# Kernel tuning notes

Hardware: AMD Instinct MI355X
Metric: run time of the kernel (lower is better)

Reference implementation:

```python
import jax, jax.numpy as jnp
import numpy as np
from math import pi

N = 20000        # nodes
E = 640000       # edges (avg degree 32)
H = 128          # hidden_channels = num_filters
NB = 3           # num_bond_features
NGS = 50 - NB    # gaussians in smearing (num_gaussians - num_bond_features)
CUT = 10.0       # cutoff
L = 3            # num_interactions
B = 16           # graphs in batch
LOG2 = 0.6931471805599453


def ssp(x):
    # ShiftedSoftplus
    return jax.nn.softplus(x) - LOG2


def setup_inputs() -> dict:
    key = jax.random.key(0)
    ks = jax.random.split(key, 20)
    s = 0.05
    inp = {
        "z": jax.random.randint(ks[0], (N,), 0, 100),
        "pos": jax.random.uniform(ks[1], (N, 3), jnp.float32),
        "batch": jnp.sort(jax.random.randint(ks[2], (N,), 0, B)),
        "edge_index": jax.random.randint(ks[3], (2, E), 0, N),
        "edge_attr": jax.random.uniform(ks[4], (E, NB), jnp.float32),
        # parameters (stacked over L interaction blocks where per-layer)
        "emb": jax.random.normal(ks[5], (100, H), jnp.float32) * s,
        "mlp_w1": jax.random.normal(ks[6], (L, NB + NGS, H), jnp.float32) * s,
        "mlp_b1": jnp.zeros((L, H), jnp.float32),
        "mlp_w2": jax.random.normal(ks[7], (L, H, H), jnp.float32) * s,
        "mlp_b2": jnp.zeros((L, H), jnp.float32),
        "cf1_w": jax.random.normal(ks[8], (L, H, H), jnp.float32) * s,   # lin1, no bias
        "cf2_w": jax.random.normal(ks[9], (L, H, H), jnp.float32) * s,
        "cf2_b": jnp.zeros((L, H), jnp.float32),
        "lin_w": jax.random.normal(ks[10], (L, H, H), jnp.float32) * s,
        "lin_b": jnp.zeros((L, H), jnp.float32),
        "out1_w": jax.random.normal(ks[11], (H, H // 2), jnp.float32) * s,
        "out1_b": jnp.zeros((H // 2,), jnp.float32),
        "out2_w": jax.random.normal(ks[12], (H // 2, 1), jnp.float32) * s,
        "out2_b": jnp.zeros((1,), jnp.float32),
    }
    return inp


def reference(z, pos, batch, edge_index, edge_attr, emb,
              mlp_w1, mlp_b1, mlp_w2, mlp_b2,
              cf1_w, cf2_w, cf2_b, lin_w, lin_b,
              out1_w, out1_b, out2_w, out2_b):
    row, col = edge_index[0], edge_index[1]  # source j, target i
    h = emb[z]                               # [N,H] embedding_e(z)
    # edge_weight = ||pos[row] - pos[col]||
    ew = jnp.linalg.norm(pos[row] - pos[col], axis=-1)  # [E]
    # GaussianSmearing(0, cutoff, NGS)
    offset = jnp.linspace(0.0, CUT, NGS, dtype=jnp.float32)
    coeff = -0.5 / (offset[1] - offset[0]) ** 2
    gs = jnp.exp(coeff * (ew[:, None] - offset[None, :]) ** 2)  # [E,NGS]
    ea = jnp.concatenate([edge_attr, gs], axis=1)  # [E,50]
    # cosine cutoff weight
    C = 0.5 * (jnp.cos(ew * pi / CUT) + 1.0)       # [E]
    for l in range(L):
        # filter MLP on edge features
        W = ssp(ea @ mlp_w1[l] + mlp_b1[l]) @ mlp_w2[l] + mlp_b2[l]  # [E,H]
        W = W * C[:, None]
        xh = h @ cf1_w[l]                    # lin1 (no bias) [N,H]
        msg = xh[row] * W                    # gather-mul [E,H]
        agg = jax.ops.segment_sum(msg, col, num_segments=N)  # scatter-add [N,H]
        xc = agg @ cf2_w[l] + cf2_b[l]       # lin2
        xc = ssp(xc)
        xc = xc @ lin_w[l] + lin_b[l]        # block output lin
        h = h + xc                           # residual
    h = ssp(h @ out1_w + out1_b)             # [N,H/2]
    per_node = h @ out2_w + out2_b           # [N,1]
    out = jax.ops.segment_sum(per_node, batch, num_segments=B)  # readout 'add' -> [B,1]
    return out
```

## Files before the change

### kernel.cpp

```cpp
#include <hip/hip_runtime.h>
#include <hip/hip_bf16.h>

typedef __attribute__((ext_vector_type(8))) short bfrag;
typedef __attribute__((ext_vector_type(4))) float f32x4;

__device__ __forceinline__ float ssp_f(float x) {
    return fmaxf(x, 0.f) + __logf(1.f + __expf(-fabsf(x))) - 0.6931471805599453f;
}

__device__ __forceinline__ unsigned short f2b(float x) {
    __hip_bfloat16 h = __float2bfloat16(x);
    return *(unsigned short*)&h;
}

__device__ __forceinline__ unsigned int pk2(float a, float b) {
    __hip_bfloat162 h2 = __float22bfloat162_rn(make_float2(a, b));
    return *(unsigned int*)&h2;
}

__device__ __forceinline__ void stage32x128(
    const float* __restrict__ src, long r0, int N, int t, short (*dst)[136])
{
    #pragma unroll
    for (int j = 0; j < 4; ++j) {
        const int fi = t + j * 256;
        const int r = fi >> 5, c4 = (fi & 31) << 2;
        const long n = r0 + r;
        float4 v = make_float4(0.f, 0.f, 0.f, 0.f);
        if (n < N) v = *(const float4*)(src + n * 128 + c4);
        *(uint2*)&dst[r][c4] = make_uint2(pk2(v.x, v.y), pk2(v.z, v.w));
    }
}

__global__ void sniff_kernel(const unsigned int* __restrict__ raw, int* __restrict__ flag)
{
    __shared__ int cnt[256];
    const int t = threadIdx.x;
    unsigned int w = raw[t];
    unsigned int e = (w >> 7) & 0xFFu;
    cnt[t] = (e >= 100u && e <= 135u) ? 1 : 0;
    __syncthreads();
    for (int s = 128; s > 0; s >>= 1) {
        if (t < s) cnt[t] += cnt[t + s];
        __syncthreads();
    }
    if (t == 0) *flag = (cnt[0] >= 160) ? 1 : 0;
}

__global__ void sniff_int_kernel(const unsigned int* __restrict__ z, int* __restrict__ iflag)
{
    __shared__ int cnt[128];
    const int t = threadIdx.x;
    cnt[t] = (z[2 * t + 1] == 0u) ? 1 : 0;
    __syncthreads();
    for (int s = 64; s > 0; s >>= 1) {
        if (t < s) cnt[t] += cnt[t + s];
        __syncthreads();
    }
    if (t == 0) *iflag = (cnt[0] >= 126) ? 1 : 0;
}

struct Cvt16 {
    const void* src[16];
    long off[17];
};

__global__ __launch_bounds__(256) void convert_fused_kernel(
    Cvt16 args, float* __restrict__ F, long total, const int* __restrict__ flag)
{
    long i = (long)blockIdx.x * 256 + threadIdx.x;
    if (i >= total) return;
    int lo = 0, hi = 16;
    while (hi - lo > 1) {
        int mid = (lo + hi) >> 1;
        if (i >= args.off[mid]) lo = mid; else hi = mid;
    }
    long loc = i - args.off[lo];
    if (*flag) F[i] = __bfloat162float(((const __hip_bfloat16*)args.src[lo])[loc]);
    else       F[i] = ((const float*)args.src[lo])[loc];
}

__global__ __launch_bounds__(256) void convert_int_kernel(
    const void* __restrict__ src, int* __restrict__ dst, int n,
    const int* __restrict__ iflag)
{
    int i = blockIdx.x * 256 + threadIdx.x;
    if (i >= n) return;
    if (*iflag) dst[i] = (int)(((const long long*)src)[i]);
    else        dst[i] = ((const int*)src)[i];
}

__global__ __launch_bounds__(256) void embed_kernel(
    const int* __restrict__ z, const float* __restrict__ embf,
    float* __restrict__ h, int NH)
{
    int idx = blockIdx.x * 256 + threadIdx.x;
    if (idx >= NH) return;
    h[idx] = embf[z[idx >> 7] * 128 + (idx & 127)];
}

__global__ __launch_bounds__(256) void zero_int_kernel(int* p, int n)
{
    int i = blockIdx.x * 256 + threadIdx.x;
    if (i < n) p[i] = 0;
}

__global__ __launch_bounds__(256) void hist_kernel(const int* __restrict__ col,
                                                   int* __restrict__ count, int E)
{
    int e = blockIdx.x * 256 + threadIdx.x;
    if (e < E) atomicAdd(&count[col[e]], 1);
}

__global__ __launch_bounds__(256) void scan_kernel(const int* __restrict__ count,
                                                   int* __restrict__ rowptr,
                                                   int* __restrict__ next, int N)
{
    __shared__ int part[256];
    const int t = threadIdx.x;
    const int chunk = (N + 255) / 256;
    const int lo = t * chunk, hi = min(lo + chunk, N);
    int s = 0;
    for (int i = lo; i < hi; ++i) s += count[i];
    part[t] = s;
    __syncthreads();
    if (t == 0) {
        int run = 0;
        for (int i = 0; i < 256; ++i) { int v = part[i]; part[i] = run; run += v; }
        rowptr[N] = run;
    }
    __syncthreads();
    int run = part[t];
    for (int i = lo; i < hi; ++i) {
        rowptr[i] = run; next[i] = run;
        run += count[i];
    }
}

__global__ __launch_bounds__(256) void prep_scatter_kernel(
    const float* __restrict__ posf, const int* __restrict__ row,
    const int* __restrict__ col, const float* __restrict__ eattrf,
    int* __restrict__ next,
    int* __restrict__ rowS, int* __restrict__ colS,
    float* __restrict__ CS, float* __restrict__ ewS,
    unsigned short* __restrict__ eaS, int E, int NB)
{
    int e = blockIdx.x * 256 + threadIdx.x;
    if (e >= E) return;
    const int r = row[e], c = col[e];
    const int p = atomicAdd(&next[c], 1);
    float dx = posf[r*3+0] - posf[c*3+0];
    float dy = posf[r*3+1] - posf[c*3+1];
    float dz = posf[r*3+2] - posf[c*3+2];
    float ew = sqrtf(dx*dx + dy*dy + dz*dz);
    rowS[p] = r; colS[p] = c; ewS[p] = ew;
    CS[p] = 0.5f * (cosf(ew * 0.3141592653589793f) + 1.0f);
    unsigned short* o = eaS + (long)p * 4;
    for (int q = 0; q < 4; ++q)
        o[q] = (q < NB) ? f2b(eattrf[(long)e * NB + q]) : (unsigned short)0;
}

__global__ __launch_bounds__(256) void wtrans_kernel(
    const float* __restrict__ src, unsigned short* __restrict__ dst,
    int K, int Kpad, int N)
{
    int idx = blockIdx.x * 256 + threadIdx.x;
    if (idx >= N * Kpad) return;
    int n = idx / Kpad, k = idx - n * Kpad;
    dst[idx] = (k < K) ? f2b(src[k * N + n]) : (unsigned short)0;
}

__global__ __launch_bounds__(256) void wtrans_node_kernel(
    const float* __restrict__ cf1, const float* __restrict__ cf2,
    const float* __restrict__ lin, unsigned short* __restrict__ dst, int total)
{
    int idx = blockIdx.x * 256 + threadIdx.x;
    if (idx >= total) return;
    int m = idx >> 14;
    int fam = m % 3, l = m / 3;
    int local = idx & 16383;
    int n = local >> 7, k = local & 127;
    const float* src = (fam == 0 ? cf1 : fam == 1 ? cf2 : lin) + (long)l * 16384;
    dst[idx] = f2b(src[k * 128 + n]);
}

template<int MODE>
__global__ __launch_bounds__(256) void node_gemm_tiled(
    const float* __restrict__ in, const float* __restrict__ W,
    const float* __restrict__ bias, float* __restrict__ out, int N)
{
    __shared__ float in_s[32][128];
    const int t = threadIdx.x;
    const long n0 = (long)blockIdx.x * 32;
    for (int i = t; i < 32 * 128; i += 256) {
        long n = n0 + (i >> 7);
        in_s[i >> 7][i & 127] = (n < N) ? in[n * 128 + (i & 127)] : 0.f;
    }
    __syncthreads();
    const int j = t & 31, sub = t >> 5;
    const int c4 = j * 4, rb = sub * 4;
    float acc[4][4];
    float4 bv = make_float4(0.f, 0.f, 0.f, 0.f);
    if (MODE != 0) bv = *(const float4*)(bias + c4);
    #pragma unroll
    for (int i = 0; i < 4; ++i) { acc[i][0]=bv.x; acc[i][1]=bv.y; acc[i][2]=bv.z; acc[i][3]=bv.w; }
    #pragma unroll 4
    for (int k = 0; k < 128; ++k) {
        const float4 wv = *(const float4*)(W + k * 128 + c4);
        #pragma unroll
        for (int i = 0; i < 4; ++i) {
            const float a = in_s[rb + i][k];
            acc[i][0] += a * wv.x; acc[i][1] += a * wv.y;
            acc[i][2] += a * wv.z; acc[i][3] += a * wv.w;
        }
    }
    #pragma unroll
    for (int i = 0; i < 4; ++i) {
        long n = n0 + rb + i;
        if (n >= N) continue;
        float4 o;
        if (MODE == 1) {
            o.x = ssp_f(acc[i][0]); o.y = ssp_f(acc[i][1]);
            o.z = ssp_f(acc[i][2]); o.w = ssp_f(acc[i][3]);
        } else {
            o.x = acc[i][0]; o.y = acc[i][1]; o.z = acc[i][2]; o.w = acc[i][3];
        }
        if (MODE == 2) {
            float4 p = *(const float4*)(out + n * 128 + c4);
            o.x += p.x; o.y += p.y; o.z += p.z; o.w += p.w;
        }
        *(float4*)(out + n * 128 + c4) = o;
    }
}

__global__ __launch_bounds__(256) void node_gemm1_mfma(
    const float* __restrict__ in, const unsigned short* __restrict__ wt,
    float* __restrict__ out, float* __restrict__ aggz, int N)
{
    __shared__ __align__(16) short a_b[32][136];
    const int t = threadIdx.x;
    const long r0 = (long)blockIdx.x * 32;
    stage32x128(in, r0, N, t, a_b);
    {
        const float4 z = make_float4(0.f, 0.f, 0.f, 0.f);
        #pragma unroll
        for (int j = 0; j < 4; ++j) {
            const int fi = t + j * 256;
            const long n = r0 + (fi >> 5);
            if (n < N) *(float4*)(aggz + n * 128 + ((fi & 31) << 2)) = z;
        }
    }
    __syncthreads();
    const int lane = t & 63, w = t >> 6;
    const int colL = lane & 15, quad = lane >> 4;
    const int rt = (w & 1) * 16 + colL;
    const int nh = (w >> 1) * 64;
    f32x4 acc[4];
    #pragma unroll
    for (int tt = 0; tt < 4; ++tt) acc[tt] = (f32x4){0.f, 0.f, 0.f, 0.f};
    #pragma unroll
    for (int ks = 0; ks < 4; ++ks) {
        const bfrag a = *(const bfrag*)&a_b[rt][ks * 32 + quad * 8];
        #pragma unroll
        for (int tt = 0; tt < 4; ++tt) {
            const bfrag wf = *(const bfrag*)&wt[(long)(nh + tt * 16 + colL) * 128 + ks * 32 + quad * 8];
            acc[tt] = __builtin_amdgcn_mfma_f32_16x16x32_bf16(wf, a, acc[tt], 0, 0, 0);
        }
    }
    const long node = r0 + rt;
    if (node < N) {
        float* orow = out + node * 128;
        #pragma unroll
        for (int tt = 0; tt < 4; ++tt) {
            const int c0 = nh + tt * 16 + quad * 4;
            *(float4*)(orow + c0) = make_float4(acc[tt][0], acc[tt][1], acc[tt][2], acc[tt][3]);
        }
    }
}

template<int CHAIN>
__global__ __launch_bounds__(256) void node_gemm23_mfma(
    const float* __restrict__ in,
    const unsigned short* __restrict__ w1t, const float* __restrict__ b1,
    const unsigned short* __restrict__ w2t, const float* __restrict__ b2,
    float* __restrict__ h,
    const unsigned short* __restrict__ cf1t, float* __restrict__ xh,
    float* __restrict__ aggz, int N)
{
    __shared__ __align__(16) short a_b[32][136];
    __shared__ __align__(16) short t_b[32][136];
    const int t = threadIdx.x;
    const long r0 = (long)blockIdx.x * 32;
    stage32x128(in, r0, N, t, a_b);
    __syncthreads();
    const int lane = t & 63, w = t >> 6;
    const int colL = lane & 15, quad = lane >> 4;
    const int rt = (w & 1) * 16 + colL;
    const int nh = (w >> 1) * 64;
    {
        f32x4 acc[4];
        #pragma unroll
        for (int tt = 0; tt < 4; ++tt) acc[tt] = (f32x4){0.f, 0.f, 0.f, 0.f};
        #pragma unroll
        for (int ks = 0; ks < 4; ++ks) {
            const bfrag a = *(const bfrag*)&a_b[rt][ks * 32 + quad * 8];
            #pragma unroll
            for (int tt = 0; tt < 4; ++tt) {
                const bfrag wf = *(const bfrag*)&w1t[(long)(nh + tt * 16 + colL) * 128 + ks * 32 + quad * 8];
                acc[tt] = __builtin_amdgcn_mfma_f32_16x16x32_bf16(wf, a, acc[tt], 0, 0, 0);
            }
        }
        #pragma unroll
        for (int tt = 0; tt < 4; ++tt) {
            const int c0 = nh + tt * 16 + quad * 4;
            const float4 bv = *(const float4*)(b1 + c0);
            const float v0 = ssp_f(acc[tt][0] + bv.x);
            const float v1 = ssp_f(acc[tt][1] + bv.y);
            const float v2 = ssp_f(acc[tt][2] + bv.z);
            const float v3 = ssp_f(acc[tt][3] + bv.w);
            *(uint2*)&t_b[rt][c0] = make_uint2(pk2(v0, v1), pk2(v2, v3));
        }
    }
    __syncthreads();
    {
        f32x4 acc[4];
        #pragma unroll
        for (int tt = 0; tt < 4; ++tt) acc[tt] = (f32x4){0.f, 0.f, 0.f, 0.f};
        #pragma unroll
        for (int ks = 0; ks < 4; ++ks) {
            const bfrag a = *(const bfrag*)&t_b[rt][ks * 32 + quad * 8];
            #pragma unroll
            for (int tt = 0; tt < 4; ++tt) {
                const bfrag wf = *(const bfrag*)&w2t[(long)(nh + tt * 16 + colL) * 128 + ks * 32 + quad * 8];
                acc[tt] = __builtin_amdgcn_mfma_f32_16x16x32_bf16(wf, a, acc[tt], 0, 0, 0);
            }
        }
        const long node = r0 + rt;
        if (node < N) {
            float* hrow = h + node * 128;
            #pragma unroll
            for (int tt = 0; tt < 4; ++tt) {
                const int c0 = nh + tt * 16 + quad * 4;
                const float4 bv = *(const float4*)(b2 + c0);
                float4 hv = *(const float4*)(hrow + c0);
                hv.x += acc[tt][0] + bv.x;
                hv.y += acc[tt][1] + bv.y;
                hv.z += acc[tt][2] + bv.z;
                hv.w += acc[tt][3] + bv.w;
                *(float4*)(hrow + c0) = hv;
                if (CHAIN)
                    *(uint2*)&a_b[rt][c0] = make_uint2(pk2(hv.x, hv.y), pk2(hv.z, hv.w));
            }
        }
    }
    if (CHAIN) {
        __syncthreads();
        f32x4 acc[4];
        #pragma unroll
        for (int tt = 0; tt < 4; ++tt) acc[tt] = (f32x4){0.f, 0.f, 0.f, 0.f};
        #pragma unroll
        for (int ks = 0; ks < 4; ++ks) {
            const bfrag a = *(const bfrag*)&a_b[rt][ks * 32 + quad * 8];
            #pragma unroll
            for (int tt = 0; tt < 4; ++tt) {
                const bfrag wf = *(const bfrag*)&cf1t[(long)(nh + tt * 16 + colL) * 128 + ks * 32 + quad * 8];
                acc[tt] = __builtin_amdgcn_mfma_f32_16x16x32_bf16(wf, a, acc[tt], 0, 0, 0);
            }
        }
        const long node = r0 + rt;
        if (node < N) {
            float* orow = xh + node * 128;
            float* zrow = aggz + node * 128;
            const float4 z = make_float4(0.f, 0.f, 0.f, 0.f);
            #pragma unroll
            for (int tt = 0; tt < 4; ++tt) {
                const int c0 = nh + tt * 16 + quad * 4;
                *(float4*)(orow + c0) = make_float4(acc[tt][0], acc[tt][1], acc[tt][2], acc[tt][3]);
                *(float4*)(zrow + c0) = z;
            }
        }
    }
}

__global__ __launch_bounds__(256, 8) void edge_mfma(
    const int* __restrict__ rowS, const int* __restrict__ colS,
    const float* __restrict__ CS, const float* __restrict__ ewS,
    const unsigned short* __restrict__ eaS,
    const unsigned short* __restrict__ w1t, const float* __restrict__ b1,
    const unsigned short* __restrict__ w2t, const float* __restrict__ b2,
    const float* __restrict__ xh, float* __restrict__ agg,
    int E, int NB, int F50, float delta, float coeff)
{
    __shared__ __align__(16) char smem[32 * 132 * 4];
    short (*ea_b)[64]    = (short(*)[64])smem;
    short (*t_b)[128]    = (short(*)[128])(smem + 4096);
    float (*runbuf)[132] = (float(*)[132])smem;
    __shared__ int   row_s[32];
    __shared__ int   col_s[32];
    __shared__ float C_s[32];
    __shared__ float ew_s[32];

    const int t = threadIdx.x;
    const long p0 = (long)blockIdx.x * 32;

    {
        const int t32 = t & 31;
        long p = p0 + t32; if (p >= E) p = E - 1;
        row_s[t32] = rowS[p];
        col_s[t32] = colS[p];
        C_s[t32]   = (p0 + t32 < E) ? CS[p] : 0.f;
        ew_s[t32]  = ewS[p];
    }
    for (int i = t; i < 32 * 64; i += 256) {
        const int e = i >> 6, k = i & 63;
        long p = p0 + e; if (p >= E) p = E - 1;
        unsigned short v;
        if (k < NB)        v = eaS[p * 4 + k];
        else if (k < F50) {
            float d = ew_s[e] - (float)(k - NB) * delta;
            v = f2b(__expf(coeff * d * d));
        } else             v = 0;
        ea_b[e][k ^ ((e & 7) << 3)] = (short)v;
    }
    __syncthreads();

    const int lane = t & 63;
    const int w    = t >> 6;
    const int colL = lane & 15;
    const int quad = lane >> 4;
    const int m0   = (w & 1) * 16;
    const int ebase = m0 + quad * 4;

    float xv[4][4];

    {
        f32x4 acc[4];
        #pragma unroll
        for (int tt = 0; tt < 4; ++tt) acc[tt] = (f32x4){0.f, 0.f, 0.f, 0.f};
        const int ar  = m0 + colL;
        const int asw = (ar & 7) << 3;
        #pragma unroll
        for (int ks = 0; ks < 2; ++ks) {
            const bfrag a = *(const bfrag*)&ea_b[ar][(ks * 32 + quad * 8) ^ asw];
            #pragma unroll
            for (int tt = 0; tt < 4; ++tt) {
                const int n0 = ((w >> 1) * 4 + tt) * 16;
                const bfrag b = *(const bfrag*)&w1t[(long)(n0 + colL) * 64 + ks * 32 + quad * 8];
                acc[tt] = __builtin_amdgcn_mfma_f32_16x16x32_bf16(a, b, acc[tt], 0, 0, 0);
            }
        }
        #pragma unroll
        for (int reg = 0; reg < 4; ++reg) {
            const float* xr = xh + (long)row_s[ebase + reg] * 128;
            #pragma unroll
            for (int tt = 0; tt < 4; ++tt)
                xv[reg][tt] = xr[((w >> 1) * 4 + tt) * 16 + colL];
        }
        #pragma unroll
        for (int tt = 0; tt < 4; ++tt) {
            const int n0 = ((w >> 1) * 4 + tt) * 16;
            const float bcol = b1[n0 + colL];
            #pragma unroll
            for (int reg = 0; reg < 4; ++reg) {
                const int rr = m0 + quad * 4 + reg;
                float v = ssp_f(acc[tt][reg] + bcol);
                t_b[rr][(n0 + colL) ^ ((rr & 7) << 3)] = (short)f2b(v);
            }
        }
    }
    __syncthreads();

    {
        f32x4 acc[4];
        #pragma unroll
        for (int tt = 0; tt < 4; ++tt) acc[tt] = (f32x4){0.f, 0.f, 0.f, 0.f};
        const int ar  = m0 + colL;
        const int asw = (ar & 7) << 3;
        #pragma unroll
        for (int ks = 0; ks < 4; ++ks) {
            const bfrag a = *(const bfrag*)&t_b[ar][(ks * 32 + quad * 8) ^ asw];
            #pragma unroll
            for (int tt = 0; tt < 4; ++tt) {
                const int n0 = ((w >> 1) * 4 + tt) * 16;
                const bfrag b = *(const bfrag*)&w2t[(long)(n0 + colL) * 128 + ks * 32 + quad * 8];
                acc[tt] = __builtin_amdgcn_mfma_f32_16x16x32_bf16(a, b, acc[tt], 0, 0, 0);
            }
        }
        __syncthreads();
        #pragma unroll
        for (int tt = 0; tt < 4; ++tt) {
            const int n0 = ((w >> 1) * 4 + tt) * 16;
            const int cg = n0 + colL;
            const float bcol = b2[cg];
            #pragma unroll
            for (int reg = 0; reg < 4; ++reg) {
                const int e = ebase + reg;
                const float v = acc[tt][reg] + bcol;
                runbuf[e][cg] = v * C_s[e] * xv[reg][tt];
            }
        }
    }
    __syncthreads();

    {
        const int cc   = t & 127;
        const int e0h  = (t >> 7) * 16;
        float a     = runbuf[e0h][cc];
        int  curcol = col_s[e0h];
        #pragma unroll 4
        for (int e = e0h + 1; e < e0h + 16; ++e) {
            const int c2 = col_s[e];
            if (c2 != curcol) {
                atomicAdd(&agg[(long)curcol * 128 + cc], a);
                a = 0.f; curcol = c2;
            }
            a += runbuf[e][cc];
        }
        atomicAdd(&agg[(long)curcol * 128 + cc], a);
    }
}

__global__ __launch_bounds__(256) void edge_atomic(
    const float* __restrict__ posf,
    const int* __restrict__ row, const int* __restrict__ col,
    const float* __restrict__ eattrf,
    const float* __restrict__ w1, const float* __restrict__ b1,
    const float* __restrict__ w2, const float* __restrict__ b2,
    const float* __restrict__ xh, float* __restrict__ agg,
    int E, int NB, int F50, float delta, float coeff)
{
    __shared__ float ea_s[32][52];
    __shared__ float t_s[32][128];
    __shared__ int   row_s[32];
    __shared__ int   col_s[32];
    __shared__ float C_s[32];
    __shared__ float ew_s[32];

    const int t = threadIdx.x;
    const long e0 = (long)blockIdx.x * 32;

    if (t < 32) {
        long e = e0 + t; if (e >= E) e = E - 1;
        const int r = row[e], c = col[e];
        row_s[t] = r; col_s[t] = c;
        float dx = posf[r*3+0] - posf[c*3+0];
        float dy = posf[r*3+1] - posf[c*3+1];
        float dz = posf[r*3+2] - posf[c*3+2];
        float ew = sqrtf(dx*dx + dy*dy + dz*dz);
        ew_s[t] = ew;
        C_s[t]  = (e0 + t < E) ? 0.5f * (cosf(ew * 0.3141592653589793f) + 1.0f) : 0.f;
        for (int q = 0; q < NB; ++q)
            ea_s[t][q] = eattrf[e * NB + q];
    }
    __syncthreads();
    {
        const int NGS = F50 - NB;
        for (int i = t; i < 32 * NGS; i += 256) {
            const int e = i / NGS, g = i - e * NGS;
            const float d = ew_s[e] - (float)g * delta;
            ea_s[e][NB + g] = __expf(coeff * d * d);
        }
    }
    __syncthreads();

    const int j = t & 31, sub = t >> 5;
    const int c4 = j * 4, eb = sub * 4;
    float acc[4][4];
    {
        const float4 bv = *(const float4*)(b1 + c4);
        #pragma unroll
        for (int i = 0; i < 4; ++i) { acc[i][0]=bv.x; acc[i][1]=bv.y; acc[i][2]=bv.z; acc[i][3]=bv.w; }
        for (int k = 0; k < F50; ++k) {
            const float4 wv = *(const float4*)(w1 + k * 128 + c4);
            #pragma unroll
            for (int i = 0; i < 4; ++i) {
                const float a = ea_s[eb + i][k];
                acc[i][0] += a * wv.x; acc[i][1] += a * wv.y;
                acc[i][2] += a * wv.z; acc[i][3] += a * wv.w;
            }
        }
        #pragma unroll
        for (int i = 0; i < 4; ++i) {
            float4 o;
            o.x = ssp_f(acc[i][0]); o.y = ssp_f(acc[i][1]);
            o.z = ssp_f(acc[i][2]); o.w = ssp_f(acc[i][3]);
            *(float4*)&t_s[eb + i][c4] = o;
        }
    }
    __syncthreads();
    {
        const float4 bv = *(const float4*)(b2 + c4);
        #pragma unroll
        for (int i = 0; i < 4; ++i) { acc[i][0]=bv.x; acc[i][1]=bv.y; acc[i][2]=bv.z; acc[i][3]=bv.w; }
        #pragma unroll 4
        for (int k = 0; k < 128; ++k) {
            const float4 wv = *(const float4*)(w2 + k * 128 + c4);
            #pragma unroll
            for (int i = 0; i < 4; ++i) {
                const float a = t_s[eb + i][k];
                acc[i][0] += a * wv.x; acc[i][1] += a * wv.y;
                acc[i][2] += a * wv.z; acc[i][3] += a * wv.w;
            }
        }
    }
    #pragma unroll
    for (int i = 0; i < 4; ++i) {
        const int e = eb + i;
        if (e0 + e >= E) continue;
        const float Ce = C_s[e];
        const float4 xv = *(const float4*)(xh + (long)row_s[e] * 128 + c4);
        float* ag = agg + (long)col_s[e] * 128 + c4;
        atomicAdd(ag + 0, acc[i][0] * Ce * xv.x);
        atomicAdd(ag + 1, acc[i][1] * Ce * xv.y);
        atomicAdd(ag + 2, acc[i][2] * Ce * xv.z);
        atomicAdd(ag + 3, acc[i][3] * Ce * xv.w);
    }
}

__global__ __launch_bounds__(256) void readout_mfma(
    const float* __restrict__ h, const unsigned short* __restrict__ o1t,
    const float* __restrict__ o1b, const float* __restrict__ o2w,
    const float* __restrict__ o2b, const int* __restrict__ batch,
    float* __restrict__ accb, int N)
{
    __shared__ __align__(16) short a_b[32][136];
    __shared__ float nb[32];
    const int t = threadIdx.x;
    const long r0 = (long)blockIdx.x * 32;
    stage32x128(h, r0, N, t, a_b);
    if (t < 32) nb[t] = 0.f;
    __syncthreads();
    const int lane = t & 63, w = t >> 6;
    const int colL = lane & 15, quad = lane >> 4;
    const int rt = (w & 1) * 16 + colL;
    const int nh = (w >> 1) * 32;
    f32x4 acc[2];
    #pragma unroll
    for (int tt = 0; tt < 2; ++tt) acc[tt] = (f32x4){0.f, 0.f, 0.f, 0.f};
    #pragma unroll
    for (int ks = 0; ks < 4; ++ks) {
        const bfrag a = *(const bfrag*)&a_b[rt][ks * 32 + quad * 8];
        #pragma unroll
        for (int tt = 0; tt < 2; ++tt) {
            const bfrag wf = *(const bfrag*)&o1t[(long)(nh + tt * 16 + colL) * 128 + ks * 32 + quad * 8];
            acc[tt] = __builtin_amdgcn_mfma_f32_16x16x32_bf16(wf, a, acc[tt], 0, 0, 0);
        }
    }
    float s = 0.f;
    #pragma unroll
    for (int tt = 0; tt < 2; ++tt) {
        const int c0 = nh + tt * 16 + quad * 4;
        const float4 bv = *(const float4*)(o1b + c0);
        const float4 wv = *(const float4*)(o2w + c0);
        s += ssp_f(acc[tt][0] + bv.x) * wv.x;
        s += ssp_f(acc[tt][1] + bv.y) * wv.y;
        s += ssp_f(acc[tt][2] + bv.z) * wv.z;
        s += ssp_f(acc[tt][3] + bv.w) * wv.w;
    }
    s += __shfl_xor(s, 16);
    s += __shfl_xor(s, 32);
    if (quad == 0) atomicAdd(&nb[rt], s);
    __syncthreads();
    if (t < 32) {
        const long node = r0 + t;
        if (node < N) atomicAdd(&accb[batch[node]], nb[t] + o2b[0]);
    }
}

__global__ __launch_bounds__(128) void readout_simple(
    const float* __restrict__ h,
    const float* __restrict__ o1w, const float* __restrict__ o1b,
    const float* __restrict__ o2w, const float* __restrict__ o2b,
    const int* __restrict__ batch, float* __restrict__ accb)
{
    __shared__ float hr[128];
    __shared__ float vv[64];
    const int n = blockIdx.x;
    const int t = threadIdx.x;
    hr[t] = h[(long)n * 128 + t];
    __syncthreads();
    if (t < 64) {
        float a = o1b[t];
        #pragma unroll 8
        for (int k = 0; k < 128; ++k)
            a = fmaf(hr[k], o1w[k * 64 + t], a);
        vv[t] = ssp_f(a) * o2w[t];
    }
    __syncthreads();
    if (t < 32) vv[t] += vv[t + 32];
    __syncthreads();
    if (t < 16) vv[t] += vv[t + 16];
    __syncthreads();
    if (t < 8)  vv[t] += vv[t + 8];
    __syncthreads();
    if (t < 4)  vv[t] += vv[t + 4];
    __syncthreads();
    if (t < 2)  vv[t] += vv[t + 2];
    __syncthreads();
    if (t == 0) atomicAdd(&accb[batch[n]], vv[0] + vv[1] + o2b[0]);
}

__global__ void finalize_kernel(const float* __restrict__ accb,
                                float* __restrict__ out, int B)
{
    int t = blockIdx.x * 256 + threadIdx.x;
    if (t < B) out[t] = accb[t];
}

extern "C" void kernel_launch(void* const* d_in, const int* in_sizes, int n_in,
                              void* d_out, int out_size, void* d_ws, size_t ws_size,
                              hipStream_t stream)
{
    const int N   = in_sizes[0];
    const int E   = in_sizes[3] / 2;
    const int B   = out_size;
    const int H   = 128;
    const int L   = in_sizes[7] / H;
    const int NB  = in_sizes[4] / E;
    const int F50 = in_sizes[6] / (L * H);
    const int NGS = F50 - NB;
    const float delta = 10.0f / (float)(NGS - 1);
    const float coeff = -0.5f / (delta * delta);

    const int fidx[16] = {1, 4, 5, 6, 7, 8, 9, 10, 11, 12, 13, 14, 15, 16, 17, 18};
    Cvt16 cv;
    cv.off[0] = 0;
    for (int i = 0; i < 16; ++i) {
        cv.src[i] = d_in[fidx[i]];
        cv.off[i + 1] = cv.off[i] + in_sizes[fidx[i]];
    }
    const long ftot = cv.off[16];

    float* F = (float*)d_ws;
    long base = (ftot + 3) & ~3L;
    float* h    = F + base;
    float* xh   = h + (long)N * H;
    float* agg  = xh + (long)N * H;
    float* accb = agg + (long)N * H;
    int*   flag  = (int*)(accb + ((B + 3) & ~3));
    int*   iflag = flag + 1;
    int*   zi     = flag + 4;
    int*   batchi = zi + N;
    int*   eidxi  = batchi + N;
    int*   count  = eidxi + 2 * E;
    int*   rowptr = count + N;
    int*   next   = rowptr + N + 1;
    int*   rowS   = next + N;
    int*   colS   = rowS + E;
    float* CS     = (float*)(colS + E);
    float* ewS    = CS + E;
    unsigned short* eaS = (unsigned short*)(ewS + E);
    unsigned short* w1t = eaS + 4L * E;
    unsigned short* w2t = w1t + (long)L * 128 * 64;
    unsigned short* nwt = w2t + (long)L * 128 * 128;
    unsigned short* o1t = nwt + 3L * L * 128 * 128;
    long used_bytes = (long)((char*)(o1t + 64 * 128) - (char*)d_ws);
    const bool use_fast = (used_bytes <= (long)ws_size) && (F50 <= 64) && (NB <= 4);

    sniff_kernel<<<1, 256, 0, stream>>>((const unsigned int*)d_in[5], flag);
    sniff_int_kernel<<<1, 128, 0, stream>>>((const unsigned int*)d_in[0], iflag);

    convert_fused_kernel<<<(int)((ftot + 255) / 256), 256, 0, stream>>>(cv, F, ftot, flag);
    convert_int_kernel<<<(N + 255) / 256, 256, 0, stream>>>(d_in[0], zi, N, iflag);
    convert_int_kernel<<<(N + 255) / 256, 256, 0, stream>>>(d_in[2], batchi, N, iflag);
    convert_int_kernel<<<(2 * E + 255) / 256, 256, 0, stream>>>(d_in[3], eidxi, 2 * E, iflag);

    const float* posf   = F + cv.off[0];
    const float* eattrf = F + cv.off[1];
    const float* embf   = F + cv.off[2];
    const float* w1   = F + cv.off[3];  const float* b1   = F + cv.off[4];
    const float* w2   = F + cv.off[5];  const float* b2   = F + cv.off[6];
    const float* cf1  = F + cv.off[7];  const float* cf2  = F + cv.off[8];
    const float* cf2b = F + cv.off[9];  const float* lin  = F + cv.off[10];
    const float* linb = F + cv.off[11]; const float* o1   = F + cv.off[12];
    const float* o1b  = F + cv.off[13]; const float* o2   = F + cv.off[14];
    const float* o2b  = F + cv.off[15];

    if (use_fast) {
        zero_int_kernel<<<(N + 255) / 256, 256, 0, stream>>>(count, N);
        hist_kernel<<<(E + 255) / 256, 256, 0, stream>>>(eidxi + E, count, E);
        scan_kernel<<<1, 256, 0, stream>>>(count, rowptr, next, N);
        prep_scatter_kernel<<<(E + 255) / 256, 256, 0, stream>>>(
            posf, eidxi, eidxi + E, eattrf, next, rowS, colS, CS, ewS, eaS, E, NB);
        for (int l = 0; l < L; ++l) {
            wtrans_kernel<<<(128 * 64 + 255) / 256, 256, 0, stream>>>(
                w1 + (long)l * F50 * H, w1t + (long)l * 128 * 64, F50, 64, 128);
            wtrans_kernel<<<(128 * 128 + 255) / 256, 256, 0, stream>>>(
                w2 + (long)l * H * H, w2t + (long)l * 128 * 128, 128, 128, 128);
        }
        const int ntot = 3 * L * 128 * 128;
        wtrans_node_kernel<<<(ntot + 255) / 256, 256, 0, stream>>>(cf1, cf2, lin, nwt, ntot);
        wtrans_kernel<<<(64 * 128 + 255) / 256, 256, 0, stream>>>(o1, o1t, 128, 128, 64);
    }

    embed_kernel<<<(N * H + 255) / 256, 256, 0, stream>>>(zi, embf, h, N * H);
    hipMemsetAsync(accb, 0, (size_t)B * sizeof(float), stream);

    const int ngemm = (N + 31) / 32;
    const int nedge = (E + 31) / 32;
    if (use_fast) {
        node_gemm1_mfma<<<ngemm, 256, 0, stream>>>(
            h, nwt + 0, xh, agg, N);
        for (int l = 0; l < L; ++l) {
            edge_mfma<<<nedge, 256, 0, stream>>>(
                rowS, colS, CS, ewS, eaS,
                w1t + (long)l * 128 * 64, b1 + (long)l * H,
                w2t + (long)l * 128 * 128, b2 + (long)l * H,
                xh, agg, E, NB, F50, delta, coeff);
            if (l < L - 1) {
                node_gemm23_mfma<1><<<ngemm, 256, 0, stream>>>(
                    agg, nwt + (long)(l * 3 + 1) * 16384, cf2b + (long)l * H,
                    nwt + (long)(l * 3 + 2) * 16384, linb + (long)l * H, h,
                    nwt + (long)((l + 1) * 3 + 0) * 16384, xh, agg, N);
            } else {
                node_gemm23_mfma<0><<<ngemm, 256, 0, stream>>>(
                    agg, nwt + (long)(l * 3 + 1) * 16384, cf2b + (long)l * H,
                    nwt + (long)(l * 3 + 2) * 16384, linb + (long)l * H, h,
                    nullptr, nullptr, nullptr, N);
            }
        }
        readout_mfma<<<ngemm, 256, 0, stream>>>(h, o1t, o1b, o2, o2b, batchi, accb, N);
    } else {
        for (int l = 0; l < L; ++l) {
            hipMemsetAsync(agg, 0, (size_t)N * H * sizeof(float), stream);
            node_gemm_tiled<0><<<ngemm, 256, 0, stream>>>(h, cf1 + (long)l * H * H, nullptr, xh, N);
            edge_atomic<<<nedge, 256, 0, stream>>>(
                posf, eidxi, eidxi + E, eattrf,
                w1 + (long)l * F50 * H, b1 + (long)l * H,
                w2 + (long)l * H * H,  b2 + (long)l * H,
                xh, agg, E, NB, F50, delta, coeff);
            node_gemm_tiled<1><<<ngemm, 256, 0, stream>>>(agg, cf2 + (long)l * H * H, cf2b + (long)l * H, xh, N);
            node_gemm_tiled<2><<<ngemm, 256, 0, stream>>>(xh, lin + (long)l * H * H, linb + (long)l * H, h, N);
        }
        readout_simple<<<N, 128, 0, stream>>>(h, o1, o1b, o2, o2b, batchi, accb);
    }
    finalize_kernel<<<(B + 255) / 256, 256, 0, stream>>>(accb, (float*)d_out, B);
}
```

Measured before the change: 1.303 ms.

## Fuse embedding into first node GEMM, halve node tiles, prefetch edge gathers

Folds the embedding lookup into the first node GEMM, which writes h and zeroes agg in the same pass, so the separate embed kernel goes away. All node GEMM and readout kernels now use 16-row tiles (more blocks, each wave computing fewer columns) to raise parallelism across the GPU. In the edge kernel, row indices and cutoff weights are loaded straight into registers, and the xh gather is issued before the MLP MFMAs so its latency can overlap with compute. The trade-off is that smaller tiles reload the weights more often per row.

```diff
diff --git a/kernel.cpp b/kernel.cpp
--- a/kernel.cpp
+++ b/kernel.cpp
@@ -16,20 +16,6 @@
 __device__ __forceinline__ unsigned int pk2(float a, float b) {
     __hip_bfloat162 h2 = __float22bfloat162_rn(make_float2(a, b));
     return *(unsigned int*)&h2;
-}
-
-__device__ __forceinline__ void stage32x128(
-    const float* __restrict__ src, long r0, int N, int t, short (*dst)[136])
-{
-    #pragma unroll
-    for (int j = 0; j < 4; ++j) {
-        const int fi = t + j * 256;
-        const int r = fi >> 5, c4 = (fi & 31) << 2;
-        const long n = r0 + r;
-        float4 v = make_float4(0.f, 0.f, 0.f, 0.f);
-        if (n < N) v = *(const float4*)(src + n * 128 + c4);
-        *(uint2*)&dst[r][c4] = make_uint2(pk2(v.x, v.y), pk2(v.z, v.w));
-    }
 }
 
 __global__ void sniff_kernel(const unsigned int* __restrict__ raw, int* __restrict__ flag)
@@ -233,45 +219,49 @@
     }
 }
 
-__global__ __launch_bounds__(256) void node_gemm1_mfma(
-    const float* __restrict__ in, const unsigned short* __restrict__ wt,
-    float* __restrict__ out, float* __restrict__ aggz, int N)
-{
-    __shared__ __align__(16) short a_b[32][136];
-    const int t = threadIdx.x;
-    const long r0 = (long)blockIdx.x * 32;
-    stage32x128(in, r0, N, t, a_b);
-    {
-        const float4 z = make_float4(0.f, 0.f, 0.f, 0.f);
-        #pragma unroll
-        for (int j = 0; j < 4; ++j) {
-            const int fi = t + j * 256;
-            const long n = r0 + (fi >> 5);
-            if (n < N) *(float4*)(aggz + n * 128 + ((fi & 31) << 2)) = z;
-        }
+__global__ __launch_bounds__(256) void node_gemm1_embed_mfma(
+    const int* __restrict__ zi, const float* __restrict__ embf,
+    const unsigned short* __restrict__ wt,
+    float* __restrict__ h, float* __restrict__ out, float* __restrict__ aggz, int N)
+{
+    __shared__ __align__(16) short a_b[16][136];
+    const int t = threadIdx.x;
+    const long r0 = (long)blockIdx.x * 16;
+    const float4 z4 = make_float4(0.f, 0.f, 0.f, 0.f);
+    #pragma unroll
+    for (int j = 0; j < 2; ++j) {
+        const int fi = t + j * 256;
+        const int r = fi >> 5, c4 = (fi & 31) << 2;
+        const long n = r0 + r;
+        float4 v = z4;
+        if (n < N) {
+            v = *(const float4*)(embf + (long)zi[n] * 128 + c4);
+            *(float4*)(h + n * 128 + c4) = v;
+            *(float4*)(aggz + n * 128 + c4) = z4;
+        }
+        *(uint2*)&a_b[r][c4] = make_uint2(pk2(v.x, v.y), pk2(v.z, v.w));
     }
     __syncthreads();
     const int lane = t & 63, w = t >> 6;
     const int colL = lane & 15, quad = lane >> 4;
-    const int rt = (w & 1) * 16 + colL;
-    const int nh = (w >> 1) * 64;
-    f32x4 acc[4];
-    #pragma unroll
-    for (int tt = 0; tt < 4; ++tt) acc[tt] = (f32x4){0.f, 0.f, 0.f, 0.f};
+    const int nh = w * 32;
+    f32x4 acc[2];
+    #pragma unroll
+    for (int tt = 0; tt < 2; ++tt) acc[tt] = (f32x4){0.f, 0.f, 0.f, 0.f};
     #pragma unroll
     for (int ks = 0; ks < 4; ++ks) {
-        const bfrag a = *(const bfrag*)&a_b[rt][ks * 32 + quad * 8];
-        #pragma unroll
-        for (int tt = 0; tt < 4; ++tt) {
+        const bfrag a = *(const bfrag*)&a_b[colL][ks * 32 + quad * 8];
+        #pragma unroll
+        for (int tt = 0; tt < 2; ++tt) {
             const bfrag wf = *(const bfrag*)&wt[(long)(nh + tt * 16 + colL) * 128 + ks * 32 + quad * 8];
             acc[tt] = __builtin_amdgcn_mfma_f32_16x16x32_bf16(wf, a, acc[tt], 0, 0, 0);
         }
     }
-    const long node = r0 + rt;
+    const long node = r0 + colL;
     if (node < N) {
         float* orow = out + node * 128;
         #pragma unroll
-        for (int tt = 0; tt < 4; ++tt) {
+        for (int tt = 0; tt < 2; ++tt) {
             const int c0 = nh + tt * 16 + quad * 4;
             *(float4*)(orow + c0) = make_float4(acc[tt][0], acc[tt][1], acc[tt][2], acc[tt][3]);
         }
@@ -287,59 +277,66 @@
     const unsigned short* __restrict__ cf1t, float* __restrict__ xh,
     float* __restrict__ aggz, int N)
 {
-    __shared__ __align__(16) short a_b[32][136];
-    __shared__ __align__(16) short t_b[32][136];
-    const int t = threadIdx.x;
-    const long r0 = (long)blockIdx.x * 32;
-    stage32x128(in, r0, N, t, a_b);
+    __shared__ __align__(16) short a_b[16][136];
+    __shared__ __align__(16) short t_b[16][136];
+    const int t = threadIdx.x;
+    const long r0 = (long)blockIdx.x * 16;
+    #pragma unroll
+    for (int j = 0; j < 2; ++j) {
+        const int fi = t + j * 256;
+        const int r = fi >> 5, c4 = (fi & 31) << 2;
+        const long n = r0 + r;
+        float4 v = make_float4(0.f, 0.f, 0.f, 0.f);
+        if (n < N) v = *(const float4*)(in + n * 128 + c4);
+        *(uint2*)&a_b[r][c4] = make_uint2(pk2(v.x, v.y), pk2(v.z, v.w));
+    }
     __syncthreads();
     const int lane = t & 63, w = t >> 6;
     const int colL = lane & 15, quad = lane >> 4;
-    const int rt = (w & 1) * 16 + colL;
-    const int nh = (w >> 1) * 64;
-    {
-        f32x4 acc[4];
-        #pragma unroll
-        for (int tt = 0; tt < 4; ++tt) acc[tt] = (f32x4){0.f, 0.f, 0.f, 0.f};
+    const int nh = w * 32;
+    {
+        f32x4 acc[2];
+        #pragma unroll
+        for (int tt = 0; tt < 2; ++tt) acc[tt] = (f32x4){0.f, 0.f, 0.f, 0.f};
         #pragma unroll
         for (int ks = 0; ks < 4; ++ks) {
-            const bfrag a = *(const bfrag*)&a_b[rt][ks * 32 + quad * 8];
-            #pragma unroll
-            for (int tt = 0; tt < 4; ++tt) {
+            const bfrag a = *(const bfrag*)&a_b[colL][ks * 32 + quad * 8];
+            #pragma unroll
+            for (int tt = 0; tt < 2; ++tt) {
                 const bfrag wf = *(const bfrag*)&w1t[(long)(nh + tt * 16 + colL) * 128 + ks * 32 + quad * 8];
                 acc[tt] = __builtin_amdgcn_mfma_f32_16x16x32_bf16(wf, a, acc[tt], 0, 0, 0);
             }
         }
         #pragma unroll
-        for (int tt = 0; tt < 4; ++tt) {
+        for (int tt = 0; tt < 2; ++tt) {
             const int c0 = nh + tt * 16 + quad * 4;
             const float4 bv = *(const float4*)(b1 + c0);
             const float v0 = ssp_f(acc[tt][0] + bv.x);
             const float v1 = ssp_f(acc[tt][1] + bv.y);
             const float v2 = ssp_f(acc[tt][2] + bv.z);
             const float v3 = ssp_f(acc[tt][3] + bv.w);
-            *(uint2*)&t_b[rt][c0] = make_uint2(pk2(v0, v1), pk2(v2, v3));
-        }
-    }
-    __syncthreads();
-    {
-        f32x4 acc[4];
-        #pragma unroll
-        for (int tt = 0; tt < 4; ++tt) acc[tt] = (f32x4){0.f, 0.f, 0.f, 0.f};
+            *(uint2*)&t_b[colL][c0] = make_uint2(pk2(v0, v1), pk2(v2, v3));
+        }
+    }
+    __syncthreads();
+    {
+        f32x4 acc[2];
+        #pragma unroll
+        for (int tt = 0; tt < 2; ++tt) acc[tt] = (f32x4){0.f, 0.f, 0.f, 0.f};
         #pragma unroll
         for (int ks = 0; ks < 4; ++ks) {
-            const bfrag a = *(const bfrag*)&t_b[rt][ks * 32 + quad * 8];
-            #pragma unroll
-            for (int tt = 0; tt < 4; ++tt) {
+            const bfrag a = *(const bfrag*)&t_b[colL][ks * 32 + quad * 8];
+            #pragma unroll
+            for (int tt = 0; tt < 2; ++tt) {
                 const bfrag wf = *(const bfrag*)&w2t[(long)(nh + tt * 16 + colL) * 128 + ks * 32 + quad * 8];
                 acc[tt] = __builtin_amdgcn_mfma_f32_16x16x32_bf16(wf, a, acc[tt], 0, 0, 0);
             }
         }
-        const long node = r0 + rt;
+        const long node = r0 + colL;
         if (node < N) {
             float* hrow = h + node * 128;
             #pragma unroll
-            for (int tt = 0; tt < 4; ++tt) {
+            for (int tt = 0; tt < 2; ++tt) {
                 const int c0 = nh + tt * 16 + quad * 4;
                 const float4 bv = *(const float4*)(b2 + c0);
                 float4 hv = *(const float4*)(hrow + c0);
@@ -349,31 +346,31 @@
                 hv.w += acc[tt][3] + bv.w;
                 *(float4*)(hrow + c0) = hv;
                 if (CHAIN)
-                    *(uint2*)&a_b[rt][c0] = make_uint2(pk2(hv.x, hv.y), pk2(hv.z, hv.w));
+                    *(uint2*)&a_b[colL][c0] = make_uint2(pk2(hv.x, hv.y), pk2(hv.z, hv.w));
             }
         }
     }
     if (CHAIN) {
         __syncthreads();
-        f32x4 acc[4];
-        #pragma unroll
-        for (int tt = 0; tt < 4; ++tt) acc[tt] = (f32x4){0.f, 0.f, 0.f, 0.f};
+        f32x4 acc[2];
+        #pragma unroll
+        for (int tt = 0; tt < 2; ++tt) acc[tt] = (f32x4){0.f, 0.f, 0.f, 0.f};
         #pragma unroll
         for (int ks = 0; ks < 4; ++ks) {
-            const bfrag a = *(const bfrag*)&a_b[rt][ks * 32 + quad * 8];
-            #pragma unroll
-            for (int tt = 0; tt < 4; ++tt) {
+            const bfrag a = *(const bfrag*)&a_b[colL][ks * 32 + quad * 8];
+            #pragma unroll
+            for (int tt = 0; tt < 2; ++tt) {
                 const bfrag wf = *(const bfrag*)&cf1t[(long)(nh + tt * 16 + colL) * 128 + ks * 32 + quad * 8];
                 acc[tt] = __builtin_amdgcn_mfma_f32_16x16x32_bf16(wf, a, acc[tt], 0, 0, 0);
             }
         }
-        const long node = r0 + rt;
+        const long node = r0 + colL;
         if (node < N) {
             float* orow = xh + node * 128;
             float* zrow = aggz + node * 128;
             const float4 z = make_float4(0.f, 0.f, 0.f, 0.f);
             #pragma unroll
-            for (int tt = 0; tt < 4; ++tt) {
+            for (int tt = 0; tt < 2; ++tt) {
                 const int c0 = nh + tt * 16 + quad * 4;
                 *(float4*)(orow + c0) = make_float4(acc[tt][0], acc[tt][1], acc[tt][2], acc[tt][3]);
                 *(float4*)(zrow + c0) = z;
@@ -395,20 +392,47 @@
     short (*ea_b)[64]    = (short(*)[64])smem;
     short (*t_b)[128]    = (short(*)[128])(smem + 4096);
     float (*runbuf)[132] = (float(*)[132])smem;
-    __shared__ int   row_s[32];
     __shared__ int   col_s[32];
-    __shared__ float C_s[32];
     __shared__ float ew_s[32];
 
     const int t = threadIdx.x;
     const long p0 = (long)blockIdx.x * 32;
+    const int lane = t & 63;
+    const int w    = t >> 6;
+    const int colL = lane & 15;
+    const int quad = lane >> 4;
+    const int m0   = (w & 1) * 16;
+    const int ebase = m0 + quad * 4;
+
+    int   row_r[4];
+    float C_r[4];
+    if (p0 + 32 <= E) {
+        const int4   rv = *(const int4*)&rowS[p0 + ebase];
+        const float4 cv = *(const float4*)&CS[p0 + ebase];
+        row_r[0] = rv.x; row_r[1] = rv.y; row_r[2] = rv.z; row_r[3] = rv.w;
+        C_r[0] = cv.x; C_r[1] = cv.y; C_r[2] = cv.z; C_r[3] = cv.w;
+    } else {
+        #pragma unroll
+        for (int reg = 0; reg < 4; ++reg) {
+            long p = p0 + ebase + reg;
+            const long pc = (p < E) ? p : E - 1;
+            row_r[reg] = rowS[pc];
+            C_r[reg]   = (p < E) ? CS[pc] : 0.f;
+        }
+    }
+    float xv[4][4];
+    #pragma unroll
+    for (int reg = 0; reg < 4; ++reg) {
+        const float* xr = xh + (long)row_r[reg] * 128;
+        #pragma unroll
+        for (int tt = 0; tt < 4; ++tt)
+            xv[reg][tt] = xr[((w >> 1) * 4 + tt) * 16 + colL];
+    }
 
     {
         const int t32 = t & 31;
         long p = p0 + t32; if (p >= E) p = E - 1;
-        row_s[t32] = rowS[p];
         col_s[t32] = colS[p];
-        C_s[t32]   = (p0 + t32 < E) ? CS[p] : 0.f;
         ew_s[t32]  = ewS[p];
     }
     for (int i = t; i < 32 * 64; i += 256) {
@@ -424,15 +448,6 @@
     }
     __syncthreads();
 
-    const int lane = t & 63;
-    const int w    = t >> 6;
-    const int colL = lane & 15;
-    const int quad = lane >> 4;
-    const int m0   = (w & 1) * 16;
-    const int ebase = m0 + quad * 4;
-
-    float xv[4][4];
-
     {
         f32x4 acc[4];
         #pragma unroll
@@ -450,13 +465,6 @@
             }
         }
         #pragma unroll
-        for (int reg = 0; reg < 4; ++reg) {
-            const float* xr = xh + (long)row_s[ebase + reg] * 128;
-            #pragma unroll
-            for (int tt = 0; tt < 4; ++tt)
-                xv[reg][tt] = xr[((w >> 1) * 4 + tt) * 16 + colL];
-        }
-        #pragma unroll
         for (int tt = 0; tt < 4; ++tt) {
             const int n0 = ((w >> 1) * 4 + tt) * 16;
             const float bcol = b1[n0 + colL];
@@ -496,7 +504,7 @@
             for (int reg = 0; reg < 4; ++reg) {
                 const int e = ebase + reg;
                 const float v = acc[tt][reg] + bcol;
-                runbuf[e][cg] = v * C_s[e] * xv[reg][tt];
+                runbuf[e][cg] = v * C_r[reg] * xv[reg][tt];
             }
         }
     }
@@ -623,45 +631,46 @@
     const float* __restrict__ o2b, const int* __restrict__ batch,
     float* __restrict__ accb, int N)
 {
-    __shared__ __align__(16) short a_b[32][136];
-    __shared__ float nb[32];
-    const int t = threadIdx.x;
-    const long r0 = (long)blockIdx.x * 32;
-    stage32x128(h, r0, N, t, a_b);
-    if (t < 32) nb[t] = 0.f;
+    __shared__ __align__(16) short a_b[16][136];
+    __shared__ float nb[16];
+    const int t = threadIdx.x;
+    const long r0 = (long)blockIdx.x * 16;
+    #pragma unroll
+    for (int j = 0; j < 2; ++j) {
+        const int fi = t + j * 256;
+        const int r = fi >> 5, c4 = (fi & 31) << 2;
+        const long n = r0 + r;
+        float4 v = make_float4(0.f, 0.f, 0.f, 0.f);
+        if (n < N) v = *(const float4*)(h + n * 128 + c4);
+        *(uint2*)&a_b[r][c4] = make_uint2(pk2(v.x, v.y), pk2(v.z, v.w));
+    }
+    if (t < 16) nb[t] = 0.f;
     __syncthreads();
     const int lane = t & 63, w = t >> 6;
     const int colL = lane & 15, quad = lane >> 4;
-    const int rt = (w & 1) * 16 + colL;
-    const int nh = (w >> 1) * 32;
-    f32x4 acc[2];
-    #pragma unroll
-    for (int tt = 0; tt < 2; ++tt) acc[tt] = (f32x4){0.f, 0.f, 0.f, 0.f};
+    const int nh = w * 16;
+    f32x4 acc = (f32x4){0.f, 0.f, 0.f, 0.f};
     #pragma unroll
     for (int ks = 0; ks < 4; ++ks) {
-        const bfrag a = *(const bfrag*)&a_b[rt][ks * 32 + quad * 8];
-        #pragma unroll
-        for (int tt = 0; tt < 2; ++tt) {
-            const bfrag wf = *(const bfrag*)&o1t[(long)(nh + tt * 16 + colL) * 128 + ks * 32 + quad * 8];
-            acc[tt] = __builtin_amdgcn_mfma_f32_16x16x32_bf16(wf, a, acc[tt], 0, 0, 0);
-        }
+        const bfrag a = *(const bfrag*)&a_b[colL][ks * 32 + quad * 8];
+        const bfrag wf = *(const bfrag*)&o1t[(long)(nh + colL) * 128 + ks * 32 + quad * 8];
+        acc = __builtin_amdgcn_mfma_f32_16x16x32_bf16(wf, a, acc, 0, 0, 0);
     }
     float s = 0.f;
-    #pragma unroll
-    for (int tt = 0; tt < 2; ++tt) {
-        const int c0 = nh + tt * 16 + quad * 4;
+    {
+        const int c0 = nh + quad * 4;
         const float4 bv = *(const float4*)(o1b + c0);
         const float4 wv = *(const float4*)(o2w + c0);
-        s += ssp_f(acc[tt][0] + bv.x) * wv.x;
-        s += ssp_f(acc[tt][1] + bv.y) * wv.y;
-        s += ssp_f(acc[tt][2] + bv.z) * wv.z;
-        s += ssp_f(acc[tt][3] + bv.w) * wv.w;
+        s += ssp_f(acc[0] + bv.x) * wv.x;
+        s += ssp_f(acc[1] + bv.y) * wv.y;
+        s += ssp_f(acc[2] + bv.z) * wv.z;
+        s += ssp_f(acc[3] + bv.w) * wv.w;
     }
     s += __shfl_xor(s, 16);
     s += __shfl_xor(s, 32);
-    if (quad == 0) atomicAdd(&nb[rt], s);
-    __syncthreads();
-    if (t < 32) {
+    if (quad == 0) atomicAdd(&nb[colL], s);
+    __syncthreads();
+    if (t < 16) {
         const long node = r0 + t;
         if (node < N) atomicAdd(&accb[batch[node]], nb[t] + o2b[0]);
     }
@@ -793,14 +802,13 @@
         wtrans_kernel<<<(64 * 128 + 255) / 256, 256, 0, stream>>>(o1, o1t, 128, 128, 64);
     }
 
-    embed_kernel<<<(N * H + 255) / 256, 256, 0, stream>>>(zi, embf, h, N * H);
     hipMemsetAsync(accb, 0, (size_t)B * sizeof(float), stream);
 
-    const int ngemm = (N + 31) / 32;
-    const int nedge = (E + 31) / 32;
+    const int ngemm16 = (N + 15) / 16;
+    const int nedge   = (E + 31) / 32;
     if (use_fast) {
-        node_gemm1_mfma<<<ngemm, 256, 0, stream>>>(
-            h, nwt + 0, xh, agg, N);
+        node_gemm1_embed_mfma<<<ngemm16, 256, 0, stream>>>(
+            zi, embf, nwt + 0, h, xh, agg, N);
         for (int l = 0; l < L; ++l) {
             edge_mfma<<<nedge, 256, 0, stream>>>(
                 rowS, colS, CS, ewS, eaS,
@@ -808,29 +816,31 @@
                 w2t + (long)l * 128 * 128, b2 + (long)l * H,
                 xh, agg, E, NB, F50, delta, coeff);
             if (l < L - 1) {
-                node_gemm23_mfma<1><<<ngemm, 256, 0, stream>>>(
+                node_gemm23_mfma<1><<<ngemm16, 256, 0, stream>>>(
                     agg, nwt + (long)(l * 3 + 1) * 16384, cf2b + (long)l * H,
                     nwt + (long)(l * 3 + 2) * 16384, linb + (long)l * H, h,
                     nwt + (long)((l + 1) * 3 + 0) * 16384, xh, agg, N);
             } else {
-                node_gemm23_mfma<0><<<ngemm, 256, 0, stream>>>(
+                node_gemm23_mfma<0><<<ngemm16, 256, 0, stream>>>(
                     agg, nwt + (long)(l * 3 + 1) * 16384, cf2b + (long)l * H,
                     nwt + (long)(l * 3 + 2) * 16384, linb + (long)l * H, h,
                     nullptr, nullptr, nullptr, N);
             }
         }
-        readout_mfma<<<ngemm, 256, 0, stream>>>(h, o1t, o1b, o2, o2b, batchi, accb, N);
+        readout_mfma<<<ngemm16, 256, 0, stream>>>(h, o1t, o1b, o2, o2b, batchi, accb, N);
     } else {
+        embed_kernel<<<(N * H + 255) / 256, 256, 0, stream>>>(zi, embf, h, N * H);
+        const int ngemm32 = (N + 31) / 32;
         for (int l = 0; l < L; ++l) {
             hipMemsetAsync(agg, 0, (size_t)N * H * sizeof(float), stream);
-            node_gemm_tiled<0><<<ngemm, 256, 0, stream>>>(h, cf1 + (long)l * H * H, nullptr, xh, N);
+            node_gemm_tiled<0><<<ngemm32, 256, 0, stream>>>(h, cf1 + (long)l * H * H, nullptr, xh, N);
             edge_atomic<<<nedge, 256, 0, stream>>>(
                 posf, eidxi, eidxi + E, eattrf,
                 w1 + (long)l * F50 * H, b1 + (long)l * H,
                 w2 + (long)l * H * H,  b2 + (long)l * H,
                 xh, agg, E, NB, F50, delta, coeff);
-            node_gemm_tiled<1><<<ngemm, 256, 0, stream>>>(agg, cf2 + (long)l * H * H, cf2b + (long)l * H, xh, N);
-            node_gemm_tiled<2><<<ngemm, 256, 0, stream>>>(xh, lin + (long)l * H * H, linb + (long)l * H, h, N);
+            node_gemm_tiled<1><<<ngemm32, 256, 0, stream>>>(agg, cf2 + (long)l * H * H, cf2b + (long)l * H, xh, N);
+            node_gemm_tiled<2><<<ngemm32, 256, 0, stream>>>(xh, lin + (long)l * H * H, linb + (long)l * H, h, N);
         }
         readout_simple<<<N, 128, 0, stream>>>(h, o1, o1b, o2, o2b, batchi, accb);
     }
```

Result: slower. 1.454 ms (+11.6%).
